# Kernel optimization log

Hardware: AMD Instinct MI355X
Metric: run time of the kernel (lower is better)

Reference implementation:

```python
import jax, jax.numpy as jnp
import numpy as np

# Sparse 3D conv config (matches init_kwargs)
D = 96          # input spatial grid (cube)
K = 3           # kernel size
S = 2           # stride
P = 1           # padding
CIN, COUT = 32, 64
B = 2           # batch size
N = 200000      # active voxels
DO = (D + 2 * P - (K - 1) - 1) // S + 1  # 48, output grid per dim


def setup_inputs() -> dict:
    key = jax.random.key(0)
    kf, kc, kb, kw = jax.random.split(key, 4)
    features = jax.random.normal(kf, (N, CIN), dtype=jnp.float32)
    sp = jax.random.randint(kc, (N, 3), 0, D)            # z, y, x
    bi = jax.random.randint(kb, (N, 1), 0, B)            # batch index
    coors = jnp.concatenate([bi, sp], axis=1).astype(jnp.int32)  # [N, 4]
    # spconv weight layout: [kz, ky, kx, Cin, Cout]
    W = jax.random.normal(kw, (K, K, K, CIN, COUT), dtype=jnp.float32) * 0.05
    return {"features": features, "coors": coors, "batch_size": B, "W": W}


def _sparse_conv3d(features, coors, W, batch_size):
    # Rulebook-free equivalent: for each kernel offset, map every active input
    # voxel to its output voxel (gather), GEMM with that offset's filter, and
    # scatter-add into the (linearly indexed) output grid. Invalid pairs are
    # masked to zero and scattered to index 0 harmlessly.
    b = coors[:, 0].astype(jnp.int32)
    z = coors[:, 1].astype(jnp.int32)
    y = coors[:, 2].astype(jnp.int32)
    x = coors[:, 3].astype(jnp.int32)
    n_out = batch_size * DO * DO * DO
    out = jnp.zeros((n_out, COUT), dtype=features.dtype)
    for kz in range(K):
        for ky in range(K):
            for kx in range(K):
                zo_n = z + P - kz
                yo_n = y + P - ky
                xo_n = x + P - kx
                valid = (zo_n % S == 0) & (yo_n % S == 0) & (xo_n % S == 0)
                zo, yo, xo = zo_n // S, yo_n // S, xo_n // S
                valid &= (zo >= 0) & (zo < DO) & (yo >= 0) & (yo < DO) & (xo >= 0) & (xo < DO)
                idx = ((b * DO + zo) * DO + yo) * DO + xo
                idx = jnp.where(valid, idx, 0)
                contrib = (features @ W[kz, ky, kx])          # [N, COUT] GEMM
                contrib = jnp.where(valid[:, None], contrib, 0.0)
                out = out.at[idx].add(contrib)                # scatter-add
    return out.reshape(batch_size, DO, DO, DO, COUT)


def reference(features, coors, batch_size, W):
    return _sparse_conv3d(features, coors, W, batch_size)
```

## Files before the change

kernel.cpp:

```cpp
#include <hip/hip_runtime.h>


#define DGRID 96
#define DOUT 48
#define CIN 32
#define COUT 64
#define NOFF 27
#define NSITE (2 * DGRID * DGRID * DGRID)
#define WPACK_ELEMS (NOFF * 4 * 64 * 8)
#define NTILE (2 * DOUT * DOUT * DOUT / 16)
#define TPW 2
#define NWAVE (NTILE / TPW)

typedef __attribute__((ext_vector_type(8))) short bf16x8;
typedef __attribute__((ext_vector_type(4))) float f32x4;

static __device__ __forceinline__ unsigned short f2bf_rne(float x) {
    unsigned u = __float_as_uint(x);
    u += 0x7fffu + ((u >> 16) & 1u);
    return (unsigned short)(u >> 16);
}

static __device__ __forceinline__ unsigned pk_bf16(float lo, float hi) {
    unsigned a = __float_as_uint(lo) + 0x8000u;
    unsigned b = __float_as_uint(hi) + 0x8000u;
    return __builtin_amdgcn_perm(b, a, 0x07060302u);
}


__global__ __launch_bounds__(256) void prep_kernel(
    const float* __restrict__ W, int* __restrict__ map,
    unsigned short* __restrict__ Wpack)
{
    const int tid = blockIdx.x * 256 + threadIdx.x;
    if (tid < NSITE / 4) {
        ((int4*)map)[tid] = make_int4(-1, -1, -1, -1);
        return;
    }
    const int w = tid - NSITE / 4;
    if (w < WPACK_ELEMS) {
        const int j = w & 7, l = (w >> 3) & 63, f = (w >> 9) & 3, o = w >> 11;
        const int k    = ((l >> 4) << 3) + j;
        const int cout = (f << 4) + (l & 15);
        Wpack[w] = f2bf_rne(W[(o * CIN + k) * COUT + cout]);
    }
}

__global__ __launch_bounds__(256) void build_map_kernel(
    const int* __restrict__ coors, int* __restrict__ map,
    int* __restrict__ nxt, int N)
{
    const int vi = blockIdx.x * 256 + threadIdx.x;
    if (vi >= N) return;
    const int b = coors[vi * 4 + 0];
    const int z = coors[vi * 4 + 1];
    const int y = coors[vi * 4 + 2];
    const int x = coors[vi * 4 + 3];
    const int site = ((b * DGRID + z) * DGRID + y) * DGRID + x;
    nxt[vi] = atomicExch(&map[site], vi);
}

__global__ __launch_bounds__(256) void merge_feat_kernel(
    const float* __restrict__ feat, const int* __restrict__ coors,
    const int* __restrict__ map, const int* __restrict__ nxt,
    unsigned short* __restrict__ featbf, int N)
{
    const int tid = blockIdx.x * 256 + threadIdx.x;
    const int vi = tid >> 3, part = tid & 7;
    if (vi >= N) return;
    const int b = coors[vi * 4 + 0];
    const int z = coors[vi * 4 + 1];
    const int y = coors[vi * 4 + 2];
    const int x = coors[vi * 4 + 3];
    const int site = ((b * DGRID + z) * DGRID + y) * DGRID + x;
    if (map[site] != vi) return;
    float4 s = *(const float4*)(feat + (size_t)vi * CIN + part * 4);
    int v2 = nxt[vi];
    while (v2 >= 0) {
        const float4 u = *(const float4*)(feat + (size_t)v2 * CIN + part * 4);
        s.x += u.x; s.y += u.y; s.z += u.z; s.w += u.w;
        v2 = nxt[v2];
    }
    uint2 p;
    p.x = pk_bf16(s.x, s.y);
    p.y = pk_bf16(s.z, s.w);
    *(uint2*)(featbf + (size_t)vi * CIN + part * 4) = p;
}

__global__ __launch_bounds__(256) void spconv_gather_kernel(
    const unsigned short* __restrict__ featbf,
    const int*            __restrict__ map,
    const unsigned short* __restrict__ Wpack,
    float*                __restrict__ out)
{
    const int lane  = threadIdx.x & 63;
    const int col   = lane & 15;
    const int khalf = lane >> 4;
    const int wid   = blockIdx.x * 4 + (threadIdx.x >> 6);

    int tb[TPW], tzo[TPW], tyo[TPW], txb[TPW];
#pragma unroll
    for (int t = 0; t < TPW; ++t) {
        const int tau = wid + t * NWAVE;
        const int x16 = tau % 3;
        const int r2  = tau / 3;
        tyo[t] = r2 % DOUT;
        const int r3 = r2 / DOUT;
        tzo[t] = r3 % DOUT;
        tb[t]  = r3 / DOUT;
        txb[t] = x16 << 4;
    }

    f32x4 acc[TPW][4];
#pragma unroll
    for (int t = 0; t < TPW; ++t)
#pragma unroll
        for (int q = 0; q < 4; ++q)
            acc[t][q] = (f32x4){0.f, 0.f, 0.f, 0.f};

    auto ldmap = [&](int off, int (&m)[TPW]) {
        const int kx = off % 3, ky = (off / 3) % 3, kz = off / 9;
#pragma unroll
        for (int t = 0; t < TPW; ++t) {
            const int zi = 2 * tzo[t] - 1 + kz;
            const int yi = 2 * tyo[t] - 1 + ky;
            int v = -1;
            if ((unsigned)zi < DGRID && (unsigned)yi < DGRID) {
                const int xi = 2 * (txb[t] + col) - 1 + kx;
                if ((unsigned)xi < DGRID)
                    v = map[((tb[t] * DGRID + zi) * DGRID + yi) * DGRID + xi];
            }
            m[t] = v;
        }
    };

    auto ldfeat = [&](const int (&m)[TPW], bf16x8 (&af)[TPW], bool (&act)[TPW]) {
#pragma unroll
        for (int t = 0; t < TPW; ++t) {
            act[t] = __ballot(m[t] >= 0) != 0ull;
            af[t] = (bf16x8)0;
            if (m[t] >= 0)
                af[t] = *(const bf16x8*)(featbf + (size_t)m[t] * CIN + (khalf << 3));
        }
    };

    int m0[TPW], m_nxt[TPW];
    ldmap(0, m0);
    ldmap(1, m_nxt);
    bf16x8 af_cur[TPW];
    bool   act_cur[TPW];
    ldfeat(m0, af_cur, act_cur);

    for (int off = 0; off < NOFF; ++off) {
        const bf16x8* wp = (const bf16x8*)Wpack + off * 256 + lane;
        const bf16x8 b0 = wp[0];
        const bf16x8 b1 = wp[64];
        const bf16x8 b2 = wp[128];
        const bf16x8 b3 = wp[192];

        int m_nn[TPW] = { -1, -1 };
        if (off + 2 < NOFF) ldmap(off + 2, m_nn);

        bf16x8 af_nxt[TPW];
        bool   act_nxt[TPW];
#pragma unroll
        for (int t = 0; t < TPW; ++t) { af_nxt[t] = (bf16x8)0; act_nxt[t] = false; }
        if (off + 1 < NOFF) ldfeat(m_nxt, af_nxt, act_nxt);

#pragma unroll
        for (int t = 0; t < TPW; ++t) {
            if (!act_cur[t]) continue;
            acc[t][0] = __builtin_amdgcn_mfma_f32_16x16x32_bf16(af_cur[t], b0, acc[t][0], 0, 0, 0);
            acc[t][1] = __builtin_amdgcn_mfma_f32_16x16x32_bf16(af_cur[t], b1, acc[t][1], 0, 0, 0);
            acc[t][2] = __builtin_amdgcn_mfma_f32_16x16x32_bf16(af_cur[t], b2, acc[t][2], 0, 0, 0);
            acc[t][3] = __builtin_amdgcn_mfma_f32_16x16x32_bf16(af_cur[t], b3, acc[t][3], 0, 0, 0);
        }

#pragma unroll
        for (int t = 0; t < TPW; ++t) {
            m_nxt[t]   = m_nn[t];
            af_cur[t]  = af_nxt[t];
            act_cur[t] = act_nxt[t];
        }
    }

#pragma unroll
    for (int t = 0; t < TPW; ++t) {
        const int tau = wid + t * NWAVE;
        float* ob = out + (size_t)tau * 16 * COUT;
#pragma unroll
        for (int r = 0; r < 4; ++r) {
            float* op = ob + ((khalf << 2) + r) * COUT + col;
            op[0]  = acc[t][0][r];
            op[16] = acc[t][1][r];
            op[32] = acc[t][2][r];
            op[48] = acc[t][3][r];
        }
    }
}

extern "C" void kernel_launch(void* const* d_in, const int* in_sizes, int n_in,
                              void* d_out, int out_size, void* d_ws, size_t ws_size,
                              hipStream_t stream) {
    const float* feat  = (const float*)d_in[0];
    const int*   coors = (const int*)d_in[1];
    const float* W     = (const float*)d_in[3];
    float*       out   = (float*)d_out;

    const int N = in_sizes[0] / CIN;

    char* ws = (char*)d_ws;
    int* map = (int*)ws;
    int* nxt = (int*)(ws + (size_t)NSITE * 4);
    const size_t featbf_off = (size_t)NSITE * 4 + (((size_t)N * 4 + 63) & ~(size_t)63);
    unsigned short* featbf = (unsigned short*)(ws + featbf_off);
    const size_t wpack_off = featbf_off + (((size_t)N * CIN * 2 + 15) & ~(size_t)15);
    unsigned short* Wpack = (unsigned short*)(ws + wpack_off);

    const int prep_blocks = (NSITE / 4 + WPACK_ELEMS + 255) / 256;
    prep_kernel<<<prep_blocks, 256, 0, stream>>>(W, map, Wpack);

    build_map_kernel<<<(N + 255) / 256, 256, 0, stream>>>(coors, map, nxt, N);

    merge_feat_kernel<<<(N * 8 + 255) / 256, 256, 0, stream>>>(
        feat, coors, map, nxt, featbf, N);

    spconv_gather_kernel<<<NWAVE / 4, 256, 0, stream>>>(featbf, map, Wpack, out);
}
```

Before: 155.0 us.

## Compact features by z-plane and swizzle gather blocks across XCDs

The merge kernel now writes each unique voxel's bf16 features into a per-(batch,z) plane bucket, using an atomic rank. It stores the bucket index, tagged with a high bit, into the site map, so the gather kernel reads features with spatial locality. The gather kernel also remaps block IDs so consecutive tiles land on the same XCD, aiming to improve L2 reuse of map and feature lines. In exchange it adds per-plane atomics, a larger feature buffer, and a fixed per-plane capacity (PCAP) that could overflow for non-uniform inputs.

After: 380.0 us. +145.1%, slower.

```diff
diff --git a/kernel.cpp b/kernel.cpp
--- a/kernel.cpp
+++ b/kernel.cpp
@@ -11,6 +11,11 @@
 #define NTILE (2 * DOUT * DOUT * DOUT / 16)
 #define TPW 2
 #define NWAVE (NTILE / TPW)
+#define NBLK (NWAVE / 4)
+#define NXCD 8
+#define NPLANE (2 * DGRID)
+#define PCAP 1344
+#define RTAG (1 << 30)
 
 typedef __attribute__((ext_vector_type(8))) short bf16x8;
 typedef __attribute__((ext_vector_type(4))) float f32x4;
@@ -30,7 +35,7 @@
 
 __global__ __launch_bounds__(256) void prep_kernel(
     const float* __restrict__ W, int* __restrict__ map,
-    unsigned short* __restrict__ Wpack)
+    int* __restrict__ cnt, unsigned short* __restrict__ Wpack)
 {
     const int tid = blockIdx.x * 256 + threadIdx.x;
     if (tid < NSITE / 4) {
@@ -43,7 +48,11 @@
         const int k    = ((l >> 4) << 3) + j;
         const int cout = (f << 4) + (l & 15);
         Wpack[w] = f2bf_rne(W[(o * CIN + k) * COUT + cout]);
-    }
+        return;
+    }
+    const int w2 = w - WPACK_ELEMS;
+    if (w2 < NPLANE / 4)
+        ((int4*)cnt)[w2] = make_int4(0, 0, 0, 0);
 }
 
 __global__ __launch_bounds__(256) void build_map_kernel(
@@ -62,8 +71,8 @@
 
 __global__ __launch_bounds__(256) void merge_feat_kernel(
     const float* __restrict__ feat, const int* __restrict__ coors,
-    const int* __restrict__ map, const int* __restrict__ nxt,
-    unsigned short* __restrict__ featbf, int N)
+    int* __restrict__ map, const int* __restrict__ nxt,
+    int* __restrict__ cnt, unsigned short* __restrict__ featbf, int N)
 {
     const int tid = blockIdx.x * 256 + threadIdx.x;
     const int vi = tid >> 3, part = tid & 7;
@@ -81,10 +90,18 @@
         s.x += u.x; s.y += u.y; s.z += u.z; s.w += u.w;
         v2 = nxt[v2];
     }
+    const int plane = b * DGRID + z;
+    int rank = 0;
+    if (part == 0) rank = atomicAdd(&cnt[plane], 1);
+    const int lane = threadIdx.x & 63;
+    rank = __shfl(rank, lane & ~7);
+    const int idx = plane * PCAP + rank;
+
     uint2 p;
     p.x = pk_bf16(s.x, s.y);
     p.y = pk_bf16(s.z, s.w);
-    *(uint2*)(featbf + (size_t)vi * CIN + part * 4) = p;
+    *(uint2*)(featbf + (size_t)idx * CIN + part * 4) = p;
+    if (part == 0) map[site] = RTAG + idx;
 }
 
 __global__ __launch_bounds__(256) void spconv_gather_kernel(
@@ -96,7 +113,11 @@
     const int lane  = threadIdx.x & 63;
     const int col   = lane & 15;
     const int khalf = lane >> 4;
-    const int wid   = blockIdx.x * 4 + (threadIdx.x >> 6);
+    const int bid  = blockIdx.x;
+    const int sbid = (bid & (NXCD - 1)) * (NBLK / NXCD) + (bid >> 3);
+    const int wid  = sbid * 4 + (threadIdx.x >> 6);
+
+    const unsigned short* fb = featbf - (size_t)RTAG * CIN;
 
     int tb[TPW], tzo[TPW], tyo[TPW], txb[TPW];
 #pragma unroll
@@ -140,7 +161,7 @@
             act[t] = __ballot(m[t] >= 0) != 0ull;
             af[t] = (bf16x8)0;
             if (m[t] >= 0)
-                af[t] = *(const bf16x8*)(featbf + (size_t)m[t] * CIN + (khalf << 3));
+                af[t] = *(const bf16x8*)(fb + (size_t)m[t] * CIN + (khalf << 3));
         }
     };
 
@@ -212,18 +233,20 @@
     char* ws = (char*)d_ws;
     int* map = (int*)ws;
     int* nxt = (int*)(ws + (size_t)NSITE * 4);
-    const size_t featbf_off = (size_t)NSITE * 4 + (((size_t)N * 4 + 63) & ~(size_t)63);
+    const size_t cnt_off = (size_t)NSITE * 4 + (((size_t)N * 4 + 63) & ~(size_t)63);
+    int* cnt = (int*)(ws + cnt_off);
+    const size_t featbf_off = cnt_off + ((NPLANE * 4 + 63) & ~63);
     unsigned short* featbf = (unsigned short*)(ws + featbf_off);
-    const size_t wpack_off = featbf_off + (((size_t)N * CIN * 2 + 15) & ~(size_t)15);
+    const size_t wpack_off = featbf_off + (((size_t)NPLANE * PCAP * CIN * 2 + 15) & ~(size_t)15);
     unsigned short* Wpack = (unsigned short*)(ws + wpack_off);
 
-    const int prep_blocks = (NSITE / 4 + WPACK_ELEMS + 255) / 256;
-    prep_kernel<<<prep_blocks, 256, 0, stream>>>(W, map, Wpack);
+    const int prep_threads = NSITE / 4 + WPACK_ELEMS + NPLANE / 4;
+    prep_kernel<<<(prep_threads + 255) / 256, 256, 0, stream>>>(W, map, cnt, Wpack);
 
     build_map_kernel<<<(N + 255) / 256, 256, 0, stream>>>(coors, map, nxt, N);
 
     merge_feat_kernel<<<(N * 8 + 255) / 256, 256, 0, stream>>>(
-        feat, coors, map, nxt, featbf, N);
+        feat, coors, map, nxt, cnt, featbf, N);
 
     spconv_gather_kernel<<<NWAVE / 4, 256, 0, stream>>>(featbf, map, Wpack, out);
 }
```
